# Kernel tuning notes

Measured on AMD Instinct MI355X. Metric: run time of the kernel, lower is better.

Reference implementation:

```python
import jax, jax.numpy as jnp
import numpy as np

N = 4096      # num nodes == lr feature dim
H = 8         # heads
HR = 256
C = 2 * HR    # heads * head_dim = 512
D = C // H    # head_dim = 64
EPS = 1e-5


def setup_inputs() -> dict:
    key = jax.random.key(0)
    ks = jax.random.split(key, 10)
    s_in = 1.0 / np.sqrt(N)
    inp = {
        "x": jax.random.normal(ks[0], (N, N), jnp.float32),
        "Wq": jax.random.normal(ks[1], (N, C), jnp.float32) * s_in,
        "bq": jax.random.normal(ks[2], (C,), jnp.float32) * 0.02,
        "Wk": jax.random.normal(ks[3], (N, C), jnp.float32) * s_in,
        "bk": jax.random.normal(ks[4], (C,), jnp.float32) * 0.02,
        "Wv": jax.random.normal(ks[5], (N, C), jnp.float32) * s_in,
        "bv": jax.random.normal(ks[6], (C,), jnp.float32) * 0.02,
        "we": jax.random.normal(ks[7], (C,), jnp.float32),
        "Wskip": jax.random.normal(ks[8], (N, C), jnp.float32) * s_in,
        "bskip": jax.random.normal(ks[9], (C,), jnp.float32) * 0.02,
        "gn_w": jnp.ones((C,), jnp.float32),
        "gn_b": jnp.zeros((C,), jnp.float32),
        "gn_ms": jnp.ones((C,), jnp.float32),
    }
    return inp


def reference(x, Wq, bq, Wk, bk, Wv, bv, we, Wskip, bskip, gn_w, gn_b, gn_ms):
    # TransformerConv on a fully-connected graph; edge (src=j -> tgt=i) attr = x[j, i].
    q = (x @ Wq + bq).reshape(N, H, D)
    k = (x @ Wk + bk).reshape(N, H, D)
    v = (x @ Wv + bv).reshape(N, H, D)
    we_h = we.reshape(H, D)                      # lin_edge weight (no bias)

    xa = x.T                                     # xa[i, j] = edge attr of j -> i
    qk = jnp.einsum('ihd,jhd->ijh', q, k)        # [N, N, H]
    qe = jnp.einsum('ihd,hd->ih', q, we_h)       # [N, H]
    scores = (qk + xa[:, :, None] * qe[:, None, :]) / jnp.sqrt(jnp.float32(D))
    alpha = jax.nn.softmax(scores, axis=1)       # softmax over sources j

    out = jnp.einsum('ijh,jhd->ihd', alpha, v)   # sum_j alpha * value_j
    s = jnp.einsum('ijh,ij->ih', alpha, xa)      # sum_j alpha * edge_attr
    out = out + s[:, :, None] * we_h[None]       # edge embedding added to value too
    out = out.reshape(N, C) + (x @ Wskip + bskip)  # root/skip connection

    # GraphNorm (single graph): per-channel stats over nodes
    mean = out.mean(axis=0)
    centered = out - gn_ms * mean
    var = jnp.mean(centered * centered, axis=0)
    out = gn_w * centered / jnp.sqrt(var + EPS) + gn_b

    # per-node L2 normalization
    out = out / jnp.sqrt(jnp.sum(out * out, axis=1, keepdims=True))
    return out
```

## Files before the change

### kernel.cpp

```cpp
#include <hip/hip_runtime.h>


typedef short s8v __attribute__((ext_vector_type(8)));
typedef unsigned short u16x8 __attribute__((ext_vector_type(8)));
typedef unsigned short u16x4 __attribute__((ext_vector_type(4)));
typedef float f4 __attribute__((ext_vector_type(4)));
typedef unsigned short u16;

__device__ __forceinline__ u16 f2bf(float f) {
    union { float f; unsigned u; } v; v.f = f;
    unsigned r = v.u + 0x7fffu + ((v.u >> 16) & 1u);
    return (u16)(r >> 16);
}
__device__ __forceinline__ u16 f2bf_hu(float f) {
    union { float f; unsigned u; } v; v.f = f;
    return (u16)((v.u + 0x8000u) >> 16);
}
__device__ __forceinline__ float bf2f(u16 h) {
    union { unsigned u; float f; } v; v.u = ((unsigned)h) << 16;
    return v.f;
}

#define GLD16(g, l) __builtin_amdgcn_global_load_lds( \
    (const __attribute__((address_space(1))) void*)(g), \
    (__attribute__((address_space(3))) void*)(l), 16, 0, 0)

__global__ __launch_bounds__(256) void k_prep(const float* __restrict__ x,
                                              const float* __restrict__ Wq,
                                              const float* __restrict__ Wk,
                                              const float* __restrict__ Wv,
                                              const float* __restrict__ Ws,
                                              u16* __restrict__ xb,
                                              u16* __restrict__ wb,
                                              float* __restrict__ stats) {
    __shared__ float tile[64][65];
    int b = blockIdx.x;
    int t = threadIdx.x;
    if (b < 8192) {
        if (b == 0) {
            stats[t] = 0.f; stats[256 + t] = 0.f; stats[512 + t] = 0.f; stats[768 + t] = 0.f;
        }
        size_t i = ((size_t)b * 256 + t) * 8;
        float4 a = *(const float4*)(x + i);
        float4 c = *(const float4*)(x + i + 4);
        u16x8 o;
        o[0]=f2bf(a.x); o[1]=f2bf(a.y); o[2]=f2bf(a.z); o[3]=f2bf(a.w);
        o[4]=f2bf(c.x); o[5]=f2bf(c.y); o[6]=f2bf(c.z); o[7]=f2bf(c.w);
        *(u16x8*)(xb + i) = o;
        return;
    }
    int bb = b - 8192;
    int k0 = (bb & 63) * 64;
    int n0 = (bb >> 6) * 64;
    const float* W = (n0 < 512) ? Wq : (n0 < 1024) ? Wk : (n0 < 1536) ? Wv : Ws;
    int col0 = n0 & 511;
#pragma unroll
    for (int q = 0; q < 4; q++) {
        int idx = t + 256 * q;
        int row = idx >> 4, c4 = (idx & 15) * 4;
        float4 v = *(const float4*)&W[(size_t)(k0 + row) * 512 + col0 + c4];
        tile[row][c4 + 0] = v.x; tile[row][c4 + 1] = v.y;
        tile[row][c4 + 2] = v.z; tile[row][c4 + 3] = v.w;
    }
    __syncthreads();
#pragma unroll
    for (int q = 0; q < 2; q++) {
        int idx = t + 256 * q;
        int row = idx >> 3, c8 = (idx & 7) * 8;
        u16x8 o;
#pragma unroll
        for (int j = 0; j < 8; j++) o[j] = f2bf(tile[c8 + j][row]);
        *(u16x8*)&wb[(size_t)(n0 + row) * 4096 + k0 + c8] = o;
    }
}

__global__ __launch_bounds__(512) void k_gemm(const u16* __restrict__ xb,
                                              const u16* __restrict__ wb,
                                              const float* __restrict__ bq,
                                              const float* __restrict__ bk,
                                              const float* __restrict__ bv,
                                              const float* __restrict__ bs,
                                              u16* __restrict__ qkvs,
                                              u16* __restrict__ vt) {
    __shared__ __align__(16) u16 A_lds[128 * 64];
    __shared__ __align__(16) u16 B_lds[128 * 64];
    int tid = threadIdx.x;
    int w = tid >> 6, lane = tid & 63;
    int wr = w >> 1, wc = w & 1;
    int L = lane & 15, q = lane >> 4;
    int m0 = blockIdx.y * 128, n0 = blockIdx.x * 128;

    const f4 fz = {0.f, 0.f, 0.f, 0.f};
    f4 acc[2][4];
#pragma unroll
    for (int r = 0; r < 2; r++)
#pragma unroll
        for (int t = 0; t < 4; t++) acc[r][t] = fz;

    int r8 = lane >> 3;
    int csw = ((lane & 7) ^ r8) * 8;
    const u16* gS;
    u16* lds_s;
    int rb0;
    if (w < 4) { gS = xb + (size_t)(m0 + r8) * 4096 + csw; lds_s = A_lds; rb0 = 32 * w; }
    else       { gS = wb + (size_t)(n0 + r8) * 4096 + csw; lds_s = B_lds; rb0 = 32 * (w - 4); }

    for (int kt = 0; kt < 64; ++kt) {
        int k0 = kt * 64;
#pragma unroll
        for (int g = 0; g < 4; g++) {
            int rb = rb0 + 8 * g;
            GLD16(gS + (size_t)rb * 4096 + k0, &lds_s[rb * 64]);
        }
        __syncthreads();
        s8v a[2][2], b[4][2];
#pragma unroll
        for (int r = 0; r < 2; r++) {
            int row = wr * 32 + 16 * r + L;
            int r7 = row & 7;
            a[r][0] = *(const s8v*)&A_lds[row * 64 + ((q ^ r7) * 8)];
            a[r][1] = *(const s8v*)&A_lds[row * 64 + (((4 + q) ^ r7) * 8)];
        }
#pragma unroll
        for (int t = 0; t < 4; t++) {
            int row = wc * 64 + 16 * t + L;
            int r7 = row & 7;
            b[t][0] = *(const s8v*)&B_lds[row * 64 + ((q ^ r7) * 8)];
            b[t][1] = *(const s8v*)&B_lds[row * 64 + (((4 + q) ^ r7) * 8)];
        }
#pragma unroll
        for (int r = 0; r < 2; r++)
#pragma unroll
            for (int t = 0; t < 4; t++) {
                acc[r][t] = __builtin_amdgcn_mfma_f32_16x16x32_bf16(a[r][0], b[t][0], acc[r][t], 0, 0, 0);
                acc[r][t] = __builtin_amdgcn_mfma_f32_16x16x32_bf16(a[r][1], b[t][1], acc[r][t], 0, 0, 0);
            }
        __syncthreads();
    }

#pragma unroll
    for (int t = 0; t < 4; t++) {
        int n = n0 + wc * 64 + 16 * t + L;
        int seg = n >> 9, o = n & 511;
        const float* bp = (seg == 0) ? bq : (seg == 1) ? bk : (seg == 2) ? bv : bs;
        float bias = bp[o];
        float scale = (seg == 0) ? 0.1803368801f : 1.f;
#pragma unroll
        for (int r = 0; r < 2; r++) {
            int mbase = m0 + wr * 32 + 16 * r + 4 * q;
            u16x4 hv;
#pragma unroll
            for (int q2 = 0; q2 < 4; q2++) {
                u16 hb = f2bf((acc[r][t][q2] + bias) * scale);
                hv[q2] = hb;
                qkvs[(size_t)(mbase + q2) * 2048 + n] = hb;
            }
            if (seg == 2)
                *(u16x4*)&vt[(size_t)(n - 1024) * 4096 + mbase] = hv;
        }
    }
}

__global__ __launch_bounds__(256, 4) void k_attn(const u16* __restrict__ qkvs,
                                                 const u16* __restrict__ xb,
                                                 const u16* __restrict__ vt,
                                                 const float* __restrict__ we,
                                                 float* __restrict__ o_part,
                                                 float* __restrict__ lsa_part) {
    __shared__ __align__(16) u16 K_lds[64 * 64];
    __shared__ __align__(16) u16 V_lds[64 * 64];
    __shared__ __align__(16) u16 P_lds[64 * 72];
    __shared__ __align__(16) u16 X_lds[64 * 72];
    __shared__ float qe8[64];

    int tid = threadIdx.x;
    int w = tid >> 6, lane = tid & 63;
    int L = lane & 15, q = lane >> 4;
    int i0 = blockIdx.x * 64;
    int h = blockIdx.y, hc = h * 64;
    int sp = blockIdx.z;

    int r8 = lane >> 3;
    int csw = ((lane & 7) ^ r8) * 8;

    {
        const u16* g0 = qkvs + (size_t)i0 * 2048 + hc;
#pragma unroll
        for (int ih = 0; ih < 2; ih++) {
            int rb = 16 * w + 8 * ih;
            GLD16(g0 + (size_t)(rb + r8) * 2048 + csw, &K_lds[rb * 64]);
        }
    }
    __syncthreads();

    s8v qf[2];
#pragma unroll
    for (int c = 0; c < 2; c++) {
        int row = 16 * w + L;
        qf[c] = *(const s8v*)&K_lds[row * 64 + (((4 * c + q) ^ (row & 7)) * 8)];
    }
    if (tid < 64) {
        float s = 0.f;
        int r7 = tid & 7;
#pragma unroll
        for (int d = 0; d < 64; d++)
            s += bf2f(K_lds[tid * 64 + ((d >> 3) ^ r7) * 8 + (d & 7)]) * we[hc + d];
        qe8[tid] = s;
    }
    __syncthreads();

    float qe_r[4];
#pragma unroll
    for (int r = 0; r < 4; r++) qe_r[r] = qe8[16 * w + 4 * q + r];

    const f4 fz = {0.f, 0.f, 0.f, 0.f};
    f4 o_acc[4];
    float l_p[4], sa_p[4];
#pragma unroll
    for (int r = 0; r < 4; r++) { l_p[r] = 0.f; sa_p[r] = 0.f; }
#pragma unroll
    for (int t = 0; t < 4; t++) o_acc[t] = fz;

    for (int jt64 = 0; jt64 < 32; ++jt64) {
        int j0 = sp * 2048 + jt64 * 64;
        {
            const u16* g0 = qkvs + (size_t)j0 * 2048 + 512 + hc;
#pragma unroll
            for (int ih = 0; ih < 2; ih++) {
                int rb = 16 * w + 8 * ih;
                GLD16(g0 + (size_t)(rb + r8) * 2048 + csw, &K_lds[rb * 64]);
            }
        }
        {
            const u16* g0 = vt + (size_t)hc * 4096 + j0;
#pragma unroll
            for (int ih = 0; ih < 2; ih++) {
                int rb = 16 * w + 8 * ih;
                GLD16(g0 + (size_t)(rb + r8) * 4096 + csw, &V_lds[rb * 64]);
            }
        }
#pragma unroll
        for (int qq = 0; qq < 2; qq++) {
            int idx = tid + 256 * qq;
            int row = idx >> 3, c8 = (idx & 7) * 8;
            *(s8v*)&X_lds[row * 72 + c8] =
                *(const s8v*)&xb[(size_t)(j0 + row) * 4096 + i0 + c8];
        }
        __syncthreads();

#pragma unroll
        for (int jt = 0; jt < 4; jt++) {
            int n = L + 16 * jt;
            int n7 = n & 7;
            s8v b0 = *(const s8v*)&K_lds[n * 64 + ((q ^ n7) * 8)];
            s8v b1 = *(const s8v*)&K_lds[n * 64 + (((4 + q) ^ n7) * 8)];
            f4 acc = fz;
            acc = __builtin_amdgcn_mfma_f32_16x16x32_bf16(qf[0], b0, acc, 0, 0, 0);
            acc = __builtin_amdgcn_mfma_f32_16x16x32_bf16(qf[1], b1, acc, 0, 0, 0);
            u16x4 xv4 = *(const u16x4*)&X_lds[n * 72 + 16 * w + 4 * q];
#pragma unroll
            for (int r = 0; r < 4; r++) {
                float xx = bf2f(xv4[r]);
                float s = fminf(acc[r] + xx * qe_r[r], 115.f);
                float p = __builtin_amdgcn_exp2f(s);
                l_p[r] += p;
                sa_p[r] += p * xx;
                P_lds[(16 * w + 4 * q + r) * 72 + n] = f2bf_hu(p);
            }
        }

        {
            int row = 16 * w + L;
            s8v a0 = *(const s8v*)&P_lds[row * 72 + q * 8];
            s8v a1 = *(const s8v*)&P_lds[row * 72 + 32 + q * 8];
#pragma unroll
            for (int t = 0; t < 4; t++) {
                int n = L + 16 * t;
                int n7 = n & 7;
                s8v b0 = *(const s8v*)&V_lds[n * 64 + ((q ^ n7) * 8)];
                s8v b1 = *(const s8v*)&V_lds[n * 64 + (((4 + q) ^ n7) * 8)];
                o_acc[t] = __builtin_amdgcn_mfma_f32_16x16x32_bf16(a0, b0, o_acc[t], 0, 0, 0);
                o_acc[t] = __builtin_amdgcn_mfma_f32_16x16x32_bf16(a1, b1, o_acc[t], 0, 0, 0);
            }
        }
        __syncthreads();
    }

#pragma unroll
    for (int r = 0; r < 4; r++) {
        float l = l_p[r], sa = sa_p[r];
        l += __shfl_xor(l, 1);  sa += __shfl_xor(sa, 1);
        l += __shfl_xor(l, 2);  sa += __shfl_xor(sa, 2);
        l += __shfl_xor(l, 4);  sa += __shfl_xor(sa, 4);
        l += __shfl_xor(l, 8);  sa += __shfl_xor(sa, 8);
        int i = i0 + 16 * w + 4 * q + r;
#pragma unroll
        for (int t = 0; t < 4; t++)
            o_part[((size_t)sp * 4096 + i) * 512 + hc + L + 16 * t] = o_acc[t][r];
        if (L == 0) {
            size_t bi = (((size_t)sp * 4096 + i) * 8 + h) * 2;
            lsa_part[bi] = l;
            lsa_part[bi + 1] = sa;
        }
    }
}

__global__ __launch_bounds__(512) void k_comb(const float* __restrict__ o_part,
                                              const float* __restrict__ lsa,
                                              const u16* __restrict__ qkvs,
                                              const float* __restrict__ we,
                                              float* __restrict__ out_pre,
                                              float* __restrict__ stats) {
    int c = threadIdx.x;
    int r0 = blockIdx.x * 64;
    int h = c >> 6;
    float wec = we[c];
    float s = 0.f, s2 = 0.f;
    for (int ii = 0; ii < 64; ii++) {
        int i = r0 + ii;
        size_t b0 = ((size_t)i * 8 + h) * 2;
        size_t b1 = (((size_t)4096 + i) * 8 + h) * 2;
        float l = lsa[b0] + lsa[b1];
        float sa = lsa[b0 + 1] + lsa[b1 + 1];
        float o = o_part[(size_t)i * 512 + c] + o_part[((size_t)4096 + i) * 512 + c];
        float inv = 1.f / l;
        float v = (o + sa * wec) * inv + bf2f(qkvs[(size_t)i * 2048 + 1536 + c]);
        out_pre[(size_t)i * 512 + c] = v;
        s += v; s2 += v * v;
    }
    atomicAdd(&stats[c], s);
    atomicAdd(&stats[512 + c], s2);
}

__global__ __launch_bounds__(512) void k_final(const float* __restrict__ out_pre,
                                               const float* __restrict__ stats,
                                               const float* __restrict__ gn_w,
                                               const float* __restrict__ gn_b,
                                               const float* __restrict__ gn_ms,
                                               float* __restrict__ out) {
    __shared__ float red[8];
    int c = threadIdx.x;
    int i = blockIdx.x;
    float mean = stats[c] * (1.f / 4096.f);
    float ex2 = stats[512 + c] * (1.f / 4096.f);
    float g = gn_ms[c];
    float var = ex2 - (2.f * g - g * g) * mean * mean;
    float y = gn_w[c] * (out_pre[(size_t)i * 512 + c] - g * mean) * rsqrtf(var + 1e-5f) + gn_b[c];
    float qv = y * y;
    qv += __shfl_xor(qv, 1);  qv += __shfl_xor(qv, 2);  qv += __shfl_xor(qv, 4);
    qv += __shfl_xor(qv, 8);  qv += __shfl_xor(qv, 16); qv += __shfl_xor(qv, 32);
    if ((c & 63) == 0) red[c >> 6] = qv;
    __syncthreads();
    float tot = 0.f;
#pragma unroll
    for (int k = 0; k < 8; k++) tot += red[k];
    out[(size_t)i * 512 + c] = y * rsqrtf(tot);
}

extern "C" void kernel_launch(void* const* d_in, const int* in_sizes, int n_in,
                              void* d_out, int out_size, void* d_ws, size_t ws_size,
                              hipStream_t stream) {
    (void)in_sizes; (void)n_in; (void)out_size; (void)ws_size;
    const float* x    = (const float*)d_in[0];
    const float* Wq   = (const float*)d_in[1];
    const float* bq   = (const float*)d_in[2];
    const float* Wk   = (const float*)d_in[3];
    const float* bk   = (const float*)d_in[4];
    const float* Wv   = (const float*)d_in[5];
    const float* bv   = (const float*)d_in[6];
    const float* we   = (const float*)d_in[7];
    const float* Ws   = (const float*)d_in[8];
    const float* bs   = (const float*)d_in[9];
    const float* gnw  = (const float*)d_in[10];
    const float* gnb  = (const float*)d_in[11];
    const float* gnms = (const float*)d_in[12];
    float* out = (float*)d_out;

    char* ws = (char*)d_ws;
    u16* xb        = (u16*)(ws);
    float* out_pre = (float*)(ws);
    u16* wb        = (u16*)(ws + (size_t)33554432);
    float* o_part  = (float*)(ws + (size_t)33554432);
    u16* qkvs      = (u16*)(ws + (size_t)50331648);
    u16* vt        = (u16*)(ws + (size_t)67108864);
    float* lsa     = (float*)(ws + (size_t)71303168);
    float* stats   = (float*)(ws + (size_t)71303168 + 524288);

    k_prep<<<10240, 256, 0, stream>>>(x, Wq, Wk, Wv, Ws, xb, wb, stats);
    k_gemm<<<dim3(16, 32), 512, 0, stream>>>(xb, wb, bq, bk, bv, bs, qkvs, vt);
    k_attn<<<dim3(64, 8, 2), 256, 0, stream>>>(qkvs, xb, vt, we, o_part, lsa);
    k_comb<<<64, 512, 0, stream>>>(o_part, lsa, qkvs, we, out_pre, stats);
    k_final<<<4096, 512, 0, stream>>>(out_pre, stats, gnw, gnb, gnms, out);
}
```

Before: 313.4 us.

## Widen attention blocks to 128 query rows sharing each K/V tile

The attention kernel now runs 512 threads per block covering 128 query rows instead of 64, so every K, V and edge-attribute tile loaded into LDS serves twice as many queries. The Q tile is staged through the enlarged P buffer, and the per-wave K/V loads are redistributed across 8 waves. This halves the number of blocks and the global K/V traffic. In exchange it raises LDS use per block, lowers block count (fewer blocks for occupancy and tail balance), and the hidden epilogue must index consistently with the wider tile.

```diff
diff --git a/kernel.cpp b/kernel.cpp
--- a/kernel.cpp
+++ b/kernel.cpp
@@ -161,7 +161,7 @@
     }
 }
 
-__global__ __launch_bounds__(256, 4) void k_attn(const u16* __restrict__ qkvs,
+__global__ __launch_bounds__(512, 4) void k_attn(const u16* __restrict__ qkvs,
                                                  const u16* __restrict__ xb,
                                                  const u16* __restrict__ vt,
                                                  const float* __restrict__ we,
@@ -169,14 +169,14 @@
                                                  float* __restrict__ lsa_part) {
     __shared__ __align__(16) u16 K_lds[64 * 64];
     __shared__ __align__(16) u16 V_lds[64 * 64];
-    __shared__ __align__(16) u16 P_lds[64 * 72];
-    __shared__ __align__(16) u16 X_lds[64 * 72];
-    __shared__ float qe8[64];
+    __shared__ __align__(16) u16 P_lds[128 * 72];
+    __shared__ __align__(16) u16 X_lds[64 * 136];
+    __shared__ float qe_s[128];
 
     int tid = threadIdx.x;
     int w = tid >> 6, lane = tid & 63;
     int L = lane & 15, q = lane >> 4;
-    int i0 = blockIdx.x * 64;
+    int i0 = blockIdx.x * 128;
     int h = blockIdx.y, hc = h * 64;
     int sp = blockIdx.z;
 
@@ -188,7 +188,7 @@
 #pragma unroll
         for (int ih = 0; ih < 2; ih++) {
             int rb = 16 * w + 8 * ih;
-            GLD16(g0 + (size_t)(rb + r8) * 2048 + csw, &K_lds[rb * 64]);
+            GLD16(g0 + (size_t)(rb + r8) * 2048 + csw, &P_lds[rb * 64]);
         }
     }
     __syncthreads();
@@ -197,21 +197,21 @@
 #pragma unroll
     for (int c = 0; c < 2; c++) {
         int row = 16 * w + L;
-        qf[c] = *(const s8v*)&K_lds[row * 64 + (((4 * c + q) ^ (row & 7)) * 8)];
-    }
-    if (tid < 64) {
+        qf[c] = *(const s8v*)&P_lds[row * 64 + (((4 * c + q) ^ (row & 7)) * 8)];
+    }
+    if (tid < 128) {
         float s = 0.f;
         int r7 = tid & 7;
 #pragma unroll
         for (int d = 0; d < 64; d++)
-            s += bf2f(K_lds[tid * 64 + ((d >> 3) ^ r7) * 8 + (d & 7)]) * we[hc + d];
-        qe8[tid] = s;
+            s += bf2f(P_lds[tid * 64 + ((d >> 3) ^ r7) * 8 + (d & 7)]) * we[hc + d];
+        qe_s[tid] = s;
     }
     __syncthreads();
 
     float qe_r[4];
 #pragma unroll
-    for (int r = 0; r < 4; r++) qe_r[r] = qe8[16 * w + 4 * q + r];
+    for (int r = 0; r < 4; r++) qe_r[r] = qe_s[16 * w + 4 * q + r];
 
     const f4 fz = {0.f, 0.f, 0.f, 0.f};
     f4 o_acc[4];
@@ -223,27 +223,13 @@
 
     for (int jt64 = 0; jt64 < 32; ++jt64) {
         int j0 = sp * 2048 + jt64 * 64;
-        {
-            const u16* g0 = qkvs + (size_t)j0 * 2048 + 512 + hc;
-#pragma unroll
-            for (int ih = 0; ih < 2; ih++) {
-                int rb = 16 * w + 8 * ih;
-                GLD16(g0 + (size_t)(rb + r8) * 2048 + csw, &K_lds[rb * 64]);
-            }
-        }
-        {
-            const u16* g0 = vt + (size_t)hc * 4096 + j0;
-#pragma unroll
-            for (int ih = 0; ih < 2; ih++) {
-                int rb = 16 * w + 8 * ih;
-                GLD16(g0 + (size_t)(rb + r8) * 4096 + csw, &V_lds[rb * 64]);
-            }
-        }
+        GLD16(qkvs + (size_t)(j0 + 8 * w + r8) * 2048 + 512 + hc + csw, &K_lds[8 * w * 64]);
+        GLD16(vt + (size_t)(hc + 8 * w + r8) * 4096 + j0 + csw, &V_lds[8 * w * 64]);
 #pragma unroll
         for (int qq = 0; qq < 2; qq++) {
-            int idx = tid + 256 * qq;
-            int row = idx >> 3, c8 = (idx & 7) * 8;
-            *(s8v*)&X_lds[row * 72 + c8] =
+            int idx = tid + 512 * qq;
+            int row = idx >> 4, c8 = (idx & 15) * 8;
+            *(s8v*)&X_lds[row * 136 + c8] =
                 *(const s8v*)&xb[(size_t)(j0 + row) * 4096 + i0 + c8];
         }
         __syncthreads();
@@ -257,7 +243,7 @@
             f4 acc = fz;
             acc = __builtin_amdgcn_mfma_f32_16x16x32_bf16(qf[0], b0, acc, 0, 0, 0);
             acc = __builtin_amdgcn_mfma_f32_16x16x32_bf16(qf[1], b1, acc, 0, 0, 0);
-            u16x4 xv4 = *(const u16x4*)&X_lds[n * 72 + 16 * w + 4 * q];
+            u16x4 xv4 = *(const u16x4*)&X_lds[n * 136 + 16 * w + 4 * q];
 #pragma unroll
             for (int r = 0; r < 4; r++) {
                 float xx = bf2f(xv4[r]);
@@ -388,7 +374,7 @@
 
     k_prep<<<10240, 256, 0, stream>>>(x, Wq, Wk, Wv, Ws, xb, wb, stats);
     k_gemm<<<dim3(16, 32), 512, 0, stream>>>(xb, wb, bq, bk, bv, bs, qkvs, vt);
-    k_attn<<<dim3(64, 8, 2), 256, 0, stream>>>(qkvs, xb, vt, we, o_part, lsa);
+    k_attn<<<dim3(32, 8, 2), 512, 0, stream>>>(qkvs, xb, vt, we, o_part, lsa);
     k_comb<<<64, 512, 0, stream>>>(o_part, lsa, qkvs, we, out_pre, stats);
     k_final<<<4096, 512, 0, stream>>>(out_pre, stats, gnw, gnb, gnms, out);
 }
```

Result: no change. 312.6 us (-0.2%).
